# Performance work log

Measured on AMD Instinct MI355X. Metric: run time of the kernel, lower is better.

The kernel has to match this reference:

```python
import jax, jax.numpy as jnp
import numpy as np

B = 256          # batch of molecules
N_ATOM = 1024    # atoms per molecule
N_EDGE = 8192    # directed edges per molecule (avg degree 8)
NEG_SLOPE = 0.01 # torch LeakyReLU default


def setup_inputs() -> dict:
    key = jax.random.key(0)
    ks = jax.random.split(key, 8)
    x = jax.random.normal(ks[0], (B, 3 * N_ATOM), dtype=jnp.float32)
    edge_index = jax.random.randint(ks[1], (2, N_EDGE), 0, N_ATOM, dtype=jnp.int64)
    # GCNConv weights (Glorot-ish small scale) and biases
    W1 = jax.random.normal(ks[2], (3, 64), dtype=jnp.float32) * 0.3
    b1 = jnp.zeros((64,), jnp.float32)
    W2 = jax.random.normal(ks[3], (64, 64), dtype=jnp.float32) * 0.1
    b2 = jnp.zeros((64,), jnp.float32)
    # project MLP: Linear(64,128) + LeakyReLU
    Wp = jax.random.normal(ks[4], (64, 128), dtype=jnp.float32) * 0.1
    bp = jnp.zeros((128,), jnp.float32)
    return {"x": x, "edge_index": edge_index, "W1": W1, "b1": b1,
            "W2": W2, "b2": b2, "Wp": Wp, "bp": bp}


def _leaky_relu(v):
    return jnp.where(v >= 0, v, NEG_SLOPE * v)


def reference(x, edge_index, W1, b1, W2, b2, Wp, bp):
    # x: [B, 3*n_atom] -> node features [B, n_atom, 3]
    bsz, n_feat = x.shape
    n = n_feat // 3
    h = x.reshape(bsz, n, 3)

    src = edge_index[0]  # message sources
    dst = edge_index[1]  # aggregation targets

    # GCN normalization with self-loops: deg[i] = 1 + in-degree(i)
    ones_e = jnp.ones((src.shape[0],), x.dtype)
    deg = jax.ops.segment_sum(ones_e, dst, num_segments=n) + 1.0
    dinv = jax.lax.rsqrt(deg)                # deg^{-1/2}, deg >= 1
    norm_e = dinv[src] * dinv[dst]           # [E]
    norm_self = dinv * dinv                  # self-loop weight per node

    def gcn(h, W, b):
        hw = h @ W                                        # [B, n, d_out]
        msg = hw[:, src, :] * norm_e[None, :, None]       # [B, E, d_out]
        agg = jax.vmap(lambda m: jax.ops.segment_sum(m, dst, num_segments=n))(msg)
        return agg + norm_self[None, :, None] * hw + b

    h = _leaky_relu(gcn(h, W1, b1))
    h = _leaky_relu(gcn(h, W2, b2))

    # global_mean_pool: every graph has exactly n atoms -> mean over atom axis
    g = h.mean(axis=1)                                    # [B, 64]

    # project MLP: Linear + LeakyReLU
    return _leaky_relu(g @ Wp + bp)                       # [B, 128]
```

## Files before the change

### kernel.cpp

```cpp
#include <hip/hip_runtime.h>

#define N_ATOMS 1024
#define N_EDGES 8192
#define NBATCH  256
#define NEG     0.01f

typedef unsigned int u32;
typedef __attribute__((ext_vector_type(8))) short bf16x8;
typedef __attribute__((ext_vector_type(4))) float f32x4;

__device__ __forceinline__ float bf_lo(u32 u) { return __uint_as_float(u << 16); }
__device__ __forceinline__ float bf_hi(u32 u) { return __uint_as_float(u & 0xffff0000u); }
__device__ __forceinline__ u32 bf_rne(float f) {
    u32 u = __float_as_uint(f);
    return (u + 0x7fffu + ((u >> 16) & 1u)) >> 16;
}
__device__ __forceinline__ u32 pack_bf(float lo, float hi) {
    return bf_rne(lo) | (bf_rne(hi) << 16);
}

#define ROWPTR_OFF 0
#define COLW_OFF   4352
#define SELFW_OFF  (4352 + 65536)
#define PERM_OFF   (4352 + 65536 + 4096)

#define TSTR_B 144
#define SM_TILE_BYTES (N_ATOMS * TSTR_B)
#define SM_CT_OFF SM_TILE_BYTES
#define SM_TOTAL (SM_TILE_BYTES + 12288)

__global__ __launch_bounds__(1024) void build_csr(
    const int* __restrict__ ei,
    int*  __restrict__ rowptr,
    int2* __restrict__ colw,
    float* __restrict__ selfw_g,
    int*  __restrict__ perm_g)
{
    __shared__ int   sdeg[N_ATOMS];
    __shared__ int   sstart[N_ATOMS];
    __shared__ float sdinv[N_ATOMS];
    __shared__ int   wtot[16];
    __shared__ int   hist[128];
    const int t = threadIdx.x;
    const int lane = t & 63;
    const int w = t >> 6;
    const int* srcA = ei;
    const int* dstA = ei + N_EDGES;

    sdeg[t] = 0;
    if (t < 128) hist[t] = 0;
    __syncthreads();
    for (int e = t; e < N_EDGES; e += 1024) atomicAdd(&sdeg[dstA[e]], 1);
    __syncthreads();

    const int myv = sdeg[t];
    int v = myv;
    #pragma unroll
    for (int d = 1; d < 64; d <<= 1) {
        int u = __shfl_up(v, d, 64);
        if (lane >= d) v += u;
    }
    if (lane == 63) wtot[w] = v;
    __syncthreads();
    if (t == 0) {
        int run = 0;
        #pragma unroll
        for (int i = 0; i < 16; ++i) { int c = wtot[i]; wtot[i] = run; run += c; }
    }
    __syncthreads();
    const int start = v - myv + wtot[w];
    sstart[t] = start;
    const float dv = rsqrtf((float)myv + 1.0f);
    sdinv[t] = dv;
    rowptr[t] = start;
    if (t == N_ATOMS - 1) rowptr[N_ATOMS] = start + myv;
    selfw_g[t] = dv * dv;

    const int dcl = myv < 127 ? myv : 127;
    atomicAdd(&hist[dcl], 1);
    sdeg[t] = 0;
    __syncthreads();
    if (t == 0) {
        int run = 0;
        for (int i = 0; i < 128; ++i) { int c = hist[i]; hist[i] = run; run += c; }
    }
    __syncthreads();
    const int pos = atomicAdd(&hist[dcl], 1);
    perm_g[pos] = t;
    __syncthreads();

    for (int e = t; e < N_EDGES; e += 1024) {
        const int d = dstA[e];
        const int s = srcA[e];
        const int slot = atomicAdd(&sdeg[d], 1);
        const float wgt = sdinv[s] * sdinv[d];
        colw[sstart[d] + slot] = make_int2(s, __float_as_int(wgt));
    }
}

__global__ __launch_bounds__(1024, 4) void gnn_main(
    const float* __restrict__ x,
    const int*  __restrict__ rowptr,
    const int2* __restrict__ colw,
    const float* __restrict__ selfw_g,
    const int*  __restrict__ perm_g,
    const float* __restrict__ W1, const float* __restrict__ b1,
    const float* __restrict__ W2, const float* __restrict__ b2,
    const float* __restrict__ Wp, const float* __restrict__ bp,
    float* __restrict__ out)
{
    extern __shared__ char smem[];
    float* ctile = (float*)(smem + SM_CT_OFF);
    float* wpool = ctile;
    float* gvec  = ctile + 1024;

    const int t = threadIdx.x;
    const int b = blockIdx.x;
    const float* xb = x + (size_t)b * (3 * N_ATOMS);

    const int atom = perm_g[t];
    const int s0 = rowptr[atom], s1 = rowptr[atom + 1];
    const float sw = selfw_g[atom];

    #pragma unroll
    for (int i = 0; i < 3; ++i) ctile[t + i * 1024] = xb[t + i * 1024];
    __syncthreads();

    {
        float A0 = sw * ctile[atom * 3 + 0];
        float A1 = sw * ctile[atom * 3 + 1];
        float A2 = sw * ctile[atom * 3 + 2];
        for (int j = s0; j < s1; ++j) {
            const int2 cw = colw[j];
            const float wt = __int_as_float(cw.y);
            const float* cr = ctile + cw.x * 3;
            A0 += wt * cr[0]; A1 += wt * cr[1]; A2 += wt * cr[2];
        }
        uint4* trow = (uint4*)(smem + (size_t)atom * TSTR_B);
        #pragma unroll
        for (int q = 0; q < 4; ++q) {
            float o[16];
            #pragma unroll
            for (int f = 0; f < 16; ++f) {
                const int fc = q * 16 + f;
                float vv = b1[fc] + A0 * W1[fc] + A1 * W1[64 + fc] + A2 * W1[128 + fc];
                o[f] = fmaxf(vv, NEG * vv);
            }
            uint4 p0, p1;
            p0.x = pack_bf(o[0],  o[1]);  p0.y = pack_bf(o[2],  o[3]);
            p0.z = pack_bf(o[4],  o[5]);  p0.w = pack_bf(o[6],  o[7]);
            p1.x = pack_bf(o[8],  o[9]);  p1.y = pack_bf(o[10], o[11]);
            p1.z = pack_bf(o[12], o[13]); p1.w = pack_bf(o[14], o[15]);
            trow[q * 2]     = p0;
            trow[q * 2 + 1] = p1;
        }
    }
    __syncthreads();

    float acc[64];
    {
        #pragma unroll
        for (int f = 0; f < 64; ++f) acc[f] = 0.0f;
        int   c  = atom;
        float wt = sw;
        for (int j = s0 - 1; j < s1; ++j) {
            const uint4* row = (const uint4*)(smem + (size_t)c * TSTR_B);
            const float wcur = wt;
            if (j + 1 < s1) {
                const int2 cw = colw[j + 1];
                c = cw.x; wt = __int_as_float(cw.y);
            }
            #pragma unroll
            for (int m = 0; m < 8; ++m) {
                const uint4 q = row[m];
                acc[8*m+0] += wcur * bf_lo(q.x);
                acc[8*m+1] += wcur * bf_hi(q.x);
                acc[8*m+2] += wcur * bf_lo(q.y);
                acc[8*m+3] += wcur * bf_hi(q.y);
                acc[8*m+4] += wcur * bf_lo(q.z);
                acc[8*m+5] += wcur * bf_hi(q.z);
                acc[8*m+6] += wcur * bf_lo(q.w);
                acc[8*m+7] += wcur * bf_hi(q.w);
            }
        }
    }
    __syncthreads();

    {
        uint4* trow = (uint4*)(smem + (size_t)atom * TSTR_B);
        #pragma unroll
        for (int q = 0; q < 8; ++q) {
            uint4 p;
            p.x = pack_bf(acc[8*q+0], acc[8*q+1]);
            p.y = pack_bf(acc[8*q+2], acc[8*q+3]);
            p.z = pack_bf(acc[8*q+4], acc[8*q+5]);
            p.w = pack_bf(acc[8*q+6], acc[8*q+7]);
            trow[q] = p;
        }
    }
    __syncthreads();

    {
        const int l15 = t & 15;
        const int lq  = (t & 63) >> 4;
        const int w   = t >> 6;

        bf16x8 wf[2][4];
        #pragma unroll
        for (int kt = 0; kt < 2; ++kt)
            #pragma unroll
            for (int ct = 0; ct < 4; ++ct)
                #pragma unroll
                for (int j = 0; j < 8; ++j) {
                    const int k = kt * 32 + lq * 8 + j;
                    wf[kt][ct][j] = (short)bf_rne(W2[k * 64 + ct * 16 + l15]);
                }
        float bias[4];
        #pragma unroll
        for (int ct = 0; ct < 4; ++ct) bias[ct] = b2[ct * 16 + l15];

        float pool[4] = {0.f, 0.f, 0.f, 0.f};
        #pragma unroll
        for (int rt = 0; rt < 4; ++rt) {
            const char* abase = smem + (size_t)(w * 64 + rt * 16 + l15) * TSTR_B + lq * 16;
            const bf16x8 a0 = *(const bf16x8*)(abase);
            const bf16x8 a1 = *(const bf16x8*)(abase + 64);
            #pragma unroll
            for (int ct = 0; ct < 4; ++ct) {
                f32x4 cf = {0.f, 0.f, 0.f, 0.f};
                cf = __builtin_amdgcn_mfma_f32_16x16x32_bf16(a0, wf[0][ct], cf, 0, 0, 0);
                cf = __builtin_amdgcn_mfma_f32_16x16x32_bf16(a1, wf[1][ct], cf, 0, 0, 0);
                float s = 0.0f;
                #pragma unroll
                for (int r = 0; r < 4; ++r) {
                    float vv = cf[r] + bias[ct];
                    s += fmaxf(vv, NEG * vv);
                }
                pool[ct] += s;
            }
        }
        #pragma unroll
        for (int ct = 0; ct < 4; ++ct) {
            pool[ct] += __shfl_xor(pool[ct], 16, 64);
            pool[ct] += __shfl_xor(pool[ct], 32, 64);
        }
        if ((t & 63) < 16) {
            #pragma unroll
            for (int ct = 0; ct < 4; ++ct)
                wpool[w * 64 + ct * 16 + l15] = pool[ct];
        }
    }
    __syncthreads();

    if (t < 64) {
        float s = 0.0f;
        #pragma unroll
        for (int w = 0; w < 16; ++w) s += wpool[w * 64 + t];
        gvec[t] = s * (1.0f / 1024.0f);
    }
    __syncthreads();

    if (t < 128) {
        float s = bp[t];
        #pragma unroll
        for (int f = 0; f < 64; ++f) s += gvec[f] * Wp[f * 128 + t];
        s = fmaxf(s, NEG * s);
        out[(size_t)b * 128 + t] = s;
    }
}

extern "C" void kernel_launch(void* const* d_in, const int* in_sizes, int n_in,
                              void* d_out, int out_size, void* d_ws, size_t ws_size,
                              hipStream_t stream) {
    const float* x  = (const float*)d_in[0];
    const int*   ei = (const int*)  d_in[1];
    const float* W1 = (const float*)d_in[2];
    const float* b1 = (const float*)d_in[3];
    const float* W2 = (const float*)d_in[4];
    const float* b2 = (const float*)d_in[5];
    const float* Wp = (const float*)d_in[6];
    const float* bp = (const float*)d_in[7];
    float* out = (float*)d_out;

    char* ws = (char*)d_ws;
    int*   rowptr = (int*)  (ws + ROWPTR_OFF);
    int2*  colw   = (int2*) (ws + COLW_OFF);
    float* selfw  = (float*)(ws + SELFW_OFF);
    int*   perm   = (int*)  (ws + PERM_OFF);

    build_csr<<<1, 1024, 0, stream>>>(ei, rowptr, colw, selfw, perm);

    (void)hipFuncSetAttribute((const void*)gnn_main,
                              hipFuncAttributeMaxDynamicSharedMemorySize, SM_TOTAL);
    gnn_main<<<NBATCH, 1024, SM_TOTAL, stream>>>(
        x, rowptr, colw, selfw, perm, W1, b1, W2, b2, Wp, bp, out);
}
```

Baseline: 43.67 us.

## Pad CSR rows to pairs, pre-pack W2, drop barrier, use packed bf16 math

Pads each CSR row to an even length with zero-weight edges so neighbor gathers load two edges per int4 and accumulate with packed f32x2 FMAs. W2 is converted and transposed to bf16 once inside build_csr, so each block loads its MFMA fragments directly instead of converting per thread. The MFMA stage now reads each wave's own permuted rows, obtained through shuffles, which lets the barrier after the layer-2 writeback be removed. Bf16 packing uses the hardware v_cvt_pk_bf16_f32 instruction, and the final projection is split across 512 threads. These cut ALU and load work in the gather loops and one block-wide sync, at the cost of extra padding edges and a more complex layout.

```diff
diff --git a/kernel.cpp b/kernel.cpp
--- a/kernel.cpp
+++ b/kernel.cpp
@@ -2,27 +2,32 @@
 
 #define N_ATOMS 1024
 #define N_EDGES 8192
+#define EPAD    (N_EDGES + N_ATOMS)
 #define NBATCH  256
 #define NEG     0.01f
 
 typedef unsigned int u32;
+typedef __attribute__((ext_vector_type(2))) float f32x2;
+typedef __attribute__((ext_vector_type(4))) float f32x4;
 typedef __attribute__((ext_vector_type(8))) short bf16x8;
-typedef __attribute__((ext_vector_type(4))) float f32x4;
-
-__device__ __forceinline__ float bf_lo(u32 u) { return __uint_as_float(u << 16); }
-__device__ __forceinline__ float bf_hi(u32 u) { return __uint_as_float(u & 0xffff0000u); }
-__device__ __forceinline__ u32 bf_rne(float f) {
-    u32 u = __float_as_uint(f);
-    return (u + 0x7fffu + ((u >> 16) & 1u)) >> 16;
-}
-__device__ __forceinline__ u32 pack_bf(float lo, float hi) {
-    return bf_rne(lo) | (bf_rne(hi) << 16);
+
+__device__ __forceinline__ u32 cvtpk(float lo, float hi) {
+    u32 r;
+    asm("v_cvt_pk_bf16_f32 %0, %1, %2" : "=v"(r) : "v"(lo), "v"(hi));
+    return r;
+}
+__device__ __forceinline__ f32x2 bfpair(u32 u) {
+    f32x2 h;
+    h.x = __uint_as_float(u << 16);
+    h.y = __uint_as_float(u & 0xffff0000u);
+    return h;
 }
 
 #define ROWPTR_OFF 0
 #define COLW_OFF   4352
-#define SELFW_OFF  (4352 + 65536)
-#define PERM_OFF   (4352 + 65536 + 4096)
+#define SELFW_OFF  (4352 + 73728)
+#define PERM_OFF   (SELFW_OFF + 4096)
+#define W2T_OFF    (PERM_OFF + 4096)
 
 #define TSTR_B 144
 #define SM_TILE_BYTES (N_ATOMS * TSTR_B)
@@ -34,7 +39,9 @@
     int*  __restrict__ rowptr,
     int2* __restrict__ colw,
     float* __restrict__ selfw_g,
-    int*  __restrict__ perm_g)
+    int*  __restrict__ perm_g,
+    u32*  __restrict__ w2t,
+    const float* __restrict__ W2)
 {
     __shared__ int   sdeg[N_ATOMS];
     __shared__ int   sstart[N_ATOMS];
@@ -49,12 +56,14 @@
 
     sdeg[t] = 0;
     if (t < 128) hist[t] = 0;
+    for (int e = t; e < EPAD; e += 1024) colw[e] = make_int2(0, 0);
     __syncthreads();
     for (int e = t; e < N_EDGES; e += 1024) atomicAdd(&sdeg[dstA[e]], 1);
     __syncthreads();
 
-    const int myv = sdeg[t];
-    int v = myv;
+    const int deg  = sdeg[t];
+    const int pdeg = (deg + 1) & ~1;
+    int v = pdeg;
     #pragma unroll
     for (int d = 1; d < 64; d <<= 1) {
         int u = __shfl_up(v, d, 64);
@@ -68,15 +77,22 @@
         for (int i = 0; i < 16; ++i) { int c = wtot[i]; wtot[i] = run; run += c; }
     }
     __syncthreads();
-    const int start = v - myv + wtot[w];
+    const int start = v - pdeg + wtot[w];
     sstart[t] = start;
-    const float dv = rsqrtf((float)myv + 1.0f);
+    const float dv = rsqrtf((float)deg + 1.0f);
     sdinv[t] = dv;
     rowptr[t] = start;
-    if (t == N_ATOMS - 1) rowptr[N_ATOMS] = start + myv;
+    if (t == N_ATOMS - 1) rowptr[N_ATOMS] = start + pdeg;
     selfw_g[t] = dv * dv;
 
-    const int dcl = myv < 127 ? myv : 127;
+    #pragma unroll
+    for (int i = 0; i < 2; ++i) {
+        const int idx = t + i * 1024;
+        const int c = idx >> 5, kk = idx & 31;
+        w2t[c * 32 + kk] = cvtpk(W2[(2 * kk) * 64 + c], W2[(2 * kk + 1) * 64 + c]);
+    }
+
+    const int dcl = deg < 127 ? deg : 127;
     atomicAdd(&hist[dcl], 1);
     sdeg[t] = 0;
     __syncthreads();
@@ -105,7 +121,7 @@
     const float* __restrict__ selfw_g,
     const int*  __restrict__ perm_g,
     const float* __restrict__ W1, const float* __restrict__ b1,
-    const float* __restrict__ W2, const float* __restrict__ b2,
+    const u32*  __restrict__ w2t, const float* __restrict__ b2,
     const float* __restrict__ Wp, const float* __restrict__ bp,
     float* __restrict__ out)
 {
@@ -113,6 +129,7 @@
     float* ctile = (float*)(smem + SM_CT_OFF);
     float* wpool = ctile;
     float* gvec  = ctile + 1024;
+    float* proj  = ctile + 1152;
 
     const int t = threadIdx.x;
     const int b = blockIdx.x;
@@ -126,79 +143,73 @@
     for (int i = 0; i < 3; ++i) ctile[t + i * 1024] = xb[t + i * 1024];
     __syncthreads();
 
+    u32 pw[32];
     {
-        float A0 = sw * ctile[atom * 3 + 0];
-        float A1 = sw * ctile[atom * 3 + 1];
-        float A2 = sw * ctile[atom * 3 + 2];
-        for (int j = s0; j < s1; ++j) {
-            const int2 cw = colw[j];
-            const float wt = __int_as_float(cw.y);
-            const float* cr = ctile + cw.x * 3;
-            A0 += wt * cr[0]; A1 += wt * cr[1]; A2 += wt * cr[2];
+        const float* crs = ctile + atom * 3;
+        float A0 = sw * crs[0], A1 = sw * crs[1], A2 = sw * crs[2];
+        for (int j = s0; j < s1; j += 2) {
+            const int4 cw = *(const int4*)(colw + j);
+            const float* c0 = ctile + cw.x * 3;
+            const float* c1 = ctile + cw.z * 3;
+            const float w0 = __int_as_float(cw.y), w1 = __int_as_float(cw.w);
+            A0 += w0 * c0[0] + w1 * c1[0];
+            A1 += w0 * c0[1] + w1 * c1[1];
+            A2 += w0 * c0[2] + w1 * c1[2];
+        }
+        #pragma unroll
+        for (int p = 0; p < 32; ++p) {
+            f32x2 vv = *(const f32x2*)(b1 + 2 * p);
+            vv = __builtin_elementwise_fma((f32x2){A0, A0}, *(const f32x2*)(W1 + 2 * p), vv);
+            vv = __builtin_elementwise_fma((f32x2){A1, A1}, *(const f32x2*)(W1 + 64 + 2 * p), vv);
+            vv = __builtin_elementwise_fma((f32x2){A2, A2}, *(const f32x2*)(W1 + 128 + 2 * p), vv);
+            vv.x = fmaxf(vv.x, NEG * vv.x);
+            vv.y = fmaxf(vv.y, NEG * vv.y);
+            pw[p] = cvtpk(vv.x, vv.y);
         }
         uint4* trow = (uint4*)(smem + (size_t)atom * TSTR_B);
         #pragma unroll
-        for (int q = 0; q < 4; ++q) {
-            float o[16];
-            #pragma unroll
-            for (int f = 0; f < 16; ++f) {
-                const int fc = q * 16 + f;
-                float vv = b1[fc] + A0 * W1[fc] + A1 * W1[64 + fc] + A2 * W1[128 + fc];
-                o[f] = fmaxf(vv, NEG * vv);
-            }
-            uint4 p0, p1;
-            p0.x = pack_bf(o[0],  o[1]);  p0.y = pack_bf(o[2],  o[3]);
-            p0.z = pack_bf(o[4],  o[5]);  p0.w = pack_bf(o[6],  o[7]);
-            p1.x = pack_bf(o[8],  o[9]);  p1.y = pack_bf(o[10], o[11]);
-            p1.z = pack_bf(o[12], o[13]); p1.w = pack_bf(o[14], o[15]);
-            trow[q * 2]     = p0;
-            trow[q * 2 + 1] = p1;
-        }
-    }
-    __syncthreads();
-
-    float acc[64];
+        for (int q = 0; q < 8; ++q)
+            trow[q] = make_uint4(pw[4 * q], pw[4 * q + 1], pw[4 * q + 2], pw[4 * q + 3]);
+    }
+    __syncthreads();
+
+    f32x2 acc[32];
     {
-        #pragma unroll
-        for (int f = 0; f < 64; ++f) acc[f] = 0.0f;
-        int   c  = atom;
-        float wt = sw;
-        for (int j = s0 - 1; j < s1; ++j) {
-            const uint4* row = (const uint4*)(smem + (size_t)c * TSTR_B);
-            const float wcur = wt;
-            if (j + 1 < s1) {
-                const int2 cw = colw[j + 1];
-                c = cw.x; wt = __int_as_float(cw.y);
-            }
+        const f32x2 sw2 = {sw, sw};
+        #pragma unroll
+        for (int p = 0; p < 32; ++p) acc[p] = bfpair(pw[p]) * sw2;
+        for (int j = s0; j < s1; j += 2) {
+            const int4 cw = *(const int4*)(colw + j);
+            const uint4* rA = (const uint4*)(smem + (size_t)cw.x * TSTR_B);
+            const uint4* rB = (const uint4*)(smem + (size_t)cw.z * TSTR_B);
+            const f32x2 wA = {__int_as_float(cw.y), __int_as_float(cw.y)};
+            const f32x2 wB = {__int_as_float(cw.w), __int_as_float(cw.w)};
             #pragma unroll
             for (int m = 0; m < 8; ++m) {
-                const uint4 q = row[m];
-                acc[8*m+0] += wcur * bf_lo(q.x);
-                acc[8*m+1] += wcur * bf_hi(q.x);
-                acc[8*m+2] += wcur * bf_lo(q.y);
-                acc[8*m+3] += wcur * bf_hi(q.y);
-                acc[8*m+4] += wcur * bf_lo(q.z);
-                acc[8*m+5] += wcur * bf_hi(q.z);
-                acc[8*m+6] += wcur * bf_lo(q.w);
-                acc[8*m+7] += wcur * bf_hi(q.w);
+                const uint4 qA = rA[m];
+                acc[4*m+0] = __builtin_elementwise_fma(bfpair(qA.x), wA, acc[4*m+0]);
+                acc[4*m+1] = __builtin_elementwise_fma(bfpair(qA.y), wA, acc[4*m+1]);
+                acc[4*m+2] = __builtin_elementwise_fma(bfpair(qA.z), wA, acc[4*m+2]);
+                acc[4*m+3] = __builtin_elementwise_fma(bfpair(qA.w), wA, acc[4*m+3]);
+                const uint4 qB = rB[m];
+                acc[4*m+0] = __builtin_elementwise_fma(bfpair(qB.x), wB, acc[4*m+0]);
+                acc[4*m+1] = __builtin_elementwise_fma(bfpair(qB.y), wB, acc[4*m+1]);
+                acc[4*m+2] = __builtin_elementwise_fma(bfpair(qB.z), wB, acc[4*m+2]);
+                acc[4*m+3] = __builtin_elementwise_fma(bfpair(qB.w), wB, acc[4*m+3]);
             }
         }
     }
     __syncthreads();
 
     {
+        u32 pb[32];
+        #pragma unroll
+        for (int p = 0; p < 32; ++p) pb[p] = cvtpk(acc[p].x, acc[p].y);
         uint4* trow = (uint4*)(smem + (size_t)atom * TSTR_B);
         #pragma unroll
-        for (int q = 0; q < 8; ++q) {
-            uint4 p;
-            p.x = pack_bf(acc[8*q+0], acc[8*q+1]);
-            p.y = pack_bf(acc[8*q+2], acc[8*q+3]);
-            p.z = pack_bf(acc[8*q+4], acc[8*q+5]);
-            p.w = pack_bf(acc[8*q+6], acc[8*q+7]);
-            trow[q] = p;
-        }
-    }
-    __syncthreads();
+        for (int q = 0; q < 8; ++q)
+            trow[q] = make_uint4(pb[4 * q], pb[4 * q + 1], pb[4 * q + 2], pb[4 * q + 3]);
+    }
 
     {
         const int l15 = t & 15;
@@ -210,11 +221,7 @@
         for (int kt = 0; kt < 2; ++kt)
             #pragma unroll
             for (int ct = 0; ct < 4; ++ct)
-                #pragma unroll
-                for (int j = 0; j < 8; ++j) {
-                    const int k = kt * 32 + lq * 8 + j;
-                    wf[kt][ct][j] = (short)bf_rne(W2[k * 64 + ct * 16 + l15]);
-                }
+                wf[kt][ct] = *(const bf16x8*)(w2t + (ct * 16 + l15) * 32 + kt * 16 + lq * 4);
         float bias[4];
         #pragma unroll
         for (int ct = 0; ct < 4; ++ct) bias[ct] = b2[ct * 16 + l15];
@@ -222,9 +229,10 @@
         float pool[4] = {0.f, 0.f, 0.f, 0.f};
         #pragma unroll
         for (int rt = 0; rt < 4; ++rt) {
-            const char* abase = smem + (size_t)(w * 64 + rt * 16 + l15) * TSTR_B + lq * 16;
-            const bf16x8 a0 = *(const bf16x8*)(abase);
-            const bf16x8 a1 = *(const bf16x8*)(abase + 64);
+            const int arow = __shfl(atom, rt * 16 + l15, 64);
+            const char* ab = smem + (size_t)arow * TSTR_B + lq * 16;
+            const bf16x8 a0 = *(const bf16x8*)(ab);
+            const bf16x8 a1 = *(const bf16x8*)(ab + 64);
             #pragma unroll
             for (int ct = 0; ct < 4; ++ct) {
                 f32x4 cf = {0.f, 0.f, 0.f, 0.f};
@@ -233,7 +241,7 @@
                 float s = 0.0f;
                 #pragma unroll
                 for (int r = 0; r < 4; ++r) {
-                    float vv = cf[r] + bias[ct];
+                    const float vv = cf[r] + bias[ct];
                     s += fmaxf(vv, NEG * vv);
                 }
                 pool[ct] += s;
@@ -259,11 +267,17 @@
         gvec[t] = s * (1.0f / 1024.0f);
     }
     __syncthreads();
-
+    if (t < 512) {
+        const int col = t & 127, pc = t >> 7;
+        float s = 0.0f;
+        #pragma unroll
+        for (int f = 0; f < 16; ++f)
+            s += gvec[pc * 16 + f] * Wp[(pc * 16 + f) * 128 + col];
+        proj[pc * 128 + col] = s;
+    }
+    __syncthreads();
     if (t < 128) {
-        float s = bp[t];
-        #pragma unroll
-        for (int f = 0; f < 64; ++f) s += gvec[f] * Wp[f * 128 + t];
+        float s = bp[t] + proj[t] + proj[128 + t] + proj[256 + t] + proj[384 + t];
         s = fmaxf(s, NEG * s);
         out[(size_t)b * 128 + t] = s;
     }
@@ -287,11 +301,12 @@
     int2*  colw   = (int2*) (ws + COLW_OFF);
     float* selfw  = (float*)(ws + SELFW_OFF);
     int*   perm   = (int*)  (ws + PERM_OFF);
-
-    build_csr<<<1, 1024, 0, stream>>>(ei, rowptr, colw, selfw, perm);
+    u32*   w2t    = (u32*)  (ws + W2T_OFF);
+
+    build_csr<<<1, 1024, 0, stream>>>(ei, rowptr, colw, selfw, perm, w2t, W2);
 
     (void)hipFuncSetAttribute((const void*)gnn_main,
                               hipFuncAttributeMaxDynamicSharedMemorySize, SM_TOTAL);
     gnn_main<<<NBATCH, 1024, SM_TOTAL, stream>>>(
-        x, rowptr, colw, selfw, perm, W1, b1, W2, b2, Wp, bp, out);
-}
+        x, rowptr, colw, selfw, perm, W1, b1, w2t, b2, Wp, bp, out);
+}
```

Result: faster. 40.89 us (-6.4%).
